# Optimization experiments

Hardware: AMD Instinct MI355X
Metric: run time of the kernel (lower is better)

The kernel has to match this reference:

```python
import jax, jax.numpy as jnp
import numpy as np

B, CIN, OUT = 16, 64, 64
CH = CIN // 2          # depthwise group count (32)
H, W = 256, 256        # mas resolution; cen is at (H//2, W//2)

# The 8 fixed 3x3 dilation-3 kernels are center-minus-shifted-neighbor ops.
# Cross-correlation offsets (dy, dx) of the -1 tap, dilation 3:
OFFSETS = [(-3, -3), (-3, 0), (-3, 3), (0, 3), (3, 3), (3, 0), (3, -3), (0, -3)]


def setup_inputs() -> dict:
    key = jax.random.key(0)
    ks = jax.random.split(key, 9)
    cen = jax.random.normal(ks[0], (B, CIN, H // 2, W // 2), jnp.float32)
    mas = jax.random.normal(ks[1], (B, CH, H, W), jnp.float32)
    # inp_layer: Conv2d(CH, CH, k=3, s=2, p=1) + SiLU
    w_inp = jax.random.normal(ks[2], (CH, CH, 3, 3), jnp.float32) * 0.05
    b_inp = jax.random.normal(ks[3], (CH,), jnp.float32) * 0.05
    # layer1/2/3: grouped 1x1, groups=CH, per-group 8 in -> 2 out; store as [CH, 2, 8]
    w1 = jax.random.normal(ks[4], (CH, 2, 8), jnp.float32) * 0.1
    w2 = jax.random.normal(ks[5], (CH, 2, 8), jnp.float32) * 0.1
    w3 = jax.random.normal(ks[6], (CH, 2, 8), jnp.float32) * 0.1
    # out_conv: 1x1 conv, 3*CIN -> OUT, with bias
    w_out = jax.random.normal(ks[7], (OUT, 3 * CIN), jnp.float32) * 0.05
    b_out = jax.random.normal(ks[8], (OUT,), jnp.float32) * 0.05
    return {"cen": cen, "mas": mas, "w_inp": w_inp, "b_inp": b_inp,
            "w1": w1, "w2": w2, "w3": w3, "w_out": w_out, "b_out": b_out}


def _forward(cen, mas, w_inp, b_inp, w1, w2, w3, w_out, b_out):
    # stem: 3x3 stride-2 conv + SiLU  -> [B, CH, H//2, W//2]
    x = jax.lax.conv_general_dilated(
        mas, w_inp, window_strides=(2, 2), padding=((1, 1), (1, 1)),
        dimension_numbers=("NCHW", "OIHW", "NCHW"))
    x = jax.nn.silu(x + b_inp[None, :, None, None])
    b, c, h, w = x.shape
    # 8 dilated depthwise diff-convs == center minus zero-padded shifted copy
    xp = jnp.pad(x, ((0, 0), (0, 0), (3, 3), (3, 3)))
    deltas = jnp.stack(
        [x - jax.lax.dynamic_slice(xp, (0, 0, 3 + dy, 3 + dx), (b, c, h, w))
         for dy, dx in OFFSETS], axis=2)                     # [B, CH, 8, h, w]
    # grouped 1x1 gating convs (groups=CH): per-group [2,8] matmul
    g1 = jnp.einsum("bcdhw,cod->bcohw", deltas, w1)
    g2 = jnp.einsum("bcdhw,cod->bcohw", deltas, w2)
    square = (g1 * g2).reshape(b, 2 * c, h, w)               # layer1 * layer2
    dout = jnp.einsum("bcdhw,cod->bcohw", deltas, w3).reshape(b, 2 * c, h, w)
    # concat [square, dout, cen] along channels -> 1x1 out_conv
    outs = jnp.concatenate([square, dout, cen], axis=1)      # [B, 3*CIN, h, w]
    return jnp.einsum("bchw,oc->bohw", outs, w_out) + b_out[None, :, None, None]


def reference(cen, mas, w_inp, b_inp, w1, w2, w3, w_out, b_out):
    return _forward(cen, mas, w_inp, b_inp, w1, w2, w3, w_out, b_out)
```

## Files before the change

kernel.cpp:

```cpp
#include <hip/hip_runtime.h>
#include <hip/hip_bf16.h>

#define BATCH 16
#define CH    32
#define CIN   64
#define OUTC  64
#define HH    128
#define WW    128
#define HW    (HH * WW)
#define MHW   65536

typedef __attribute__((ext_vector_type(8))) short bf16x8;
typedef __attribute__((ext_vector_type(4))) float f32x4;

__device__ inline unsigned short bf16u(float x) {
  union { __hip_bfloat16 h; unsigned short s; } u;
  u.h = __float2bfloat16(x);
  return u.s;
}
__device__ inline unsigned int pack2(float lo, float hi) {
  return (unsigned int)bf16u(lo) | ((unsigned int)bf16u(hi) << 16);
}
__device__ inline float losf(unsigned u) { return __uint_as_float(u << 16); }
__device__ inline float hisf(unsigned u) { return __uint_as_float(u & 0xffff0000u); }

__global__ __launch_bounds__(256) void k_prep_weights(
    const float* __restrict__ w_out, const float* __restrict__ w_inp,
    const float* __restrict__ w3,
    unsigned short* __restrict__ wfrag, unsigned short* __restrict__ wfrag2,
    unsigned short* __restrict__ wfrag3) {
  int t = blockIdx.x * 256 + threadIdx.x;
  if (t < 9 * 2 * 64 * 8) {
    int e    = t & 7;
    int lane = (t >> 3) & 63;
    int ct   = (t >> 9) & 1;
    int tap  = t >> 10;
    int co = ct * 16 + (lane & 15);
    int ci = (lane >> 4) * 8 + e;
    wfrag[t] = bf16u(w_inp[(co * CH + ci) * 9 + tap]);
  }
  int t2 = t - 9216;
  if (t2 >= 0 && t2 < 8192) {
    int e    = t2 & 7;
    int lane = (t2 >> 3) & 63;
    int ot   = (t2 >> 9) & 3;
    int kt   = t2 >> 11;
    int o = ot * 16 + (lane & 15);
    int k = kt * 32 + (lane >> 4) * 8 + e;
    int col = (k < 64) ? k : 64 + k;
    wfrag2[t2] = bf16u(w_out[o * 192 + col]);
  }
  int t3 = t - 17408;
  if (t3 >= 0 && t3 < 18432) {
    int e    = t3 & 7;
    int lane = (t3 >> 3) & 63;
    int ot   = (t3 >> 9) & 3;
    int tap  = t3 >> 11;
    int o = ot * 16 + (lane & 15);
    int C = (lane >> 4) * 8 + e;
    const int kmap[9] = {0, 1, 2, 7, -1, 3, 6, 5, 4};
    float v = 0.f;
    if (tap == 4) {
      for (int k = 0; k < 8; ++k)
        for (int op = 0; op < 2; ++op)
          v += w_out[o * 192 + 64 + 2 * C + op] * w3[C * 16 + op * 8 + k];
    } else {
      int k = kmap[tap];
      for (int op = 0; op < 2; ++op)
        v -= w_out[o * 192 + 64 + 2 * C + op] * w3[C * 16 + op * 8 + k];
    }
    wfrag3[t3] = bf16u(v);
  }
}

__global__ __launch_bounds__(256, 6) void k_stem(
    const float* __restrict__ mas, const unsigned short* __restrict__ wfrag,
    const float* __restrict__ b_inp, unsigned short* __restrict__ xbuf) {
  __shared__ alignas(16) unsigned int xs32[325 * 18];

  const int W = blockIdx.x + 4 * blockIdx.y + 256 * blockIdx.z;
  const int F = (W & 7) * 512 + (W >> 3);
  const int bx = F & 3;
  const int by = (F >> 2) & 63;
  const int b  = F >> 8;

  const int t  = threadIdx.x;
  const int lane = t & 63;
  const int w = t >> 6;

  const int I0 = by * 2, J0 = bx * 32;
  const int R0 = 4 * by - 1, C0 = 64 * bx - 1;

  const float* mb = mas + (size_t)b * CH * MHW;

  if (R0 >= 0) {
#pragma unroll 5
    for (int idx = t; idx < 2560; idx += 256) {
      int cell = idx >> 5;
      int k    = idx & 31;
      int r  = cell >> 4;
      int cp = cell & 15;
      const float* p = mb + (size_t)(2 * cp) * MHW +
                       (size_t)(R0 + r) * 256 + (C0 + 1 + 2 * k);
      float2 a = *(const float2*)(p);
      float2 c = *(const float2*)(p + MHW);
      int base = (r * 65 + 1 + 2 * k) * 18 + cp;
      xs32[base]      = pack2(a.x, c.x);
      xs32[base + 18] = pack2(a.y, c.y);
    }
  } else {
#pragma unroll 5
    for (int idx = t; idx < 2560; idx += 256) {
      int cell = idx >> 5;
      int k    = idx & 31;
      int r  = cell >> 4;
      int cp = cell & 15;
      int gr = R0 + r;
      unsigned v0 = 0u, v1 = 0u;
      if (gr >= 0) {
        const float* p = mb + (size_t)(2 * cp) * MHW + (size_t)gr * 256 +
                         (C0 + 1 + 2 * k);
        float2 a = *(const float2*)(p);
        float2 c = *(const float2*)(p + MHW);
        v0 = pack2(a.x, c.x);
        v1 = pack2(a.y, c.y);
      }
      int base = (r * 65 + 1 + 2 * k) * 18 + cp;
      xs32[base]      = v0;
      xs32[base + 18] = v1;
    }
  }
  if (t < 80) {
    int r = t >> 4, cp = t & 15;
    int gr = R0 + r;
    unsigned v = 0u;
    if (gr >= 0 && bx > 0) {
      const float* p = mb + (size_t)(2 * cp) * MHW + (size_t)gr * 256 + C0;
      v = pack2(p[0], p[MHW]);
    }
    xs32[(r * 65) * 18 + cp] = v;
  }
  __syncthreads();

  const int il = w >> 1, h = w & 1;
  const int jl = lane & 15;
  const int g4 = (lane >> 4) * 4;
  const int tc = h * 16 + jl;

  f32x4 acc[2];
  acc[0] = 0.f;
  acc[1] = 0.f;

  const bf16x8* wf = (const bf16x8*)wfrag;
#pragma unroll
  for (int ky = 0; ky < 3; ++ky) {
#pragma unroll
    for (int kx = 0; kx < 3; ++kx) {
      const int tap = ky * 3 + kx;
      bf16x8 a0 = wf[(tap * 2 + 0) * 64 + lane];
      bf16x8 a1 = wf[(tap * 2 + 1) * 64 + lane];
      int pix = (2 * il + ky) * 65 + 2 * tc + kx;
      bf16x8 bfr = *(const bf16x8*)(xs32 + pix * 18 + g4);
      acc[0] = __builtin_amdgcn_mfma_f32_16x16x32_bf16(a0, bfr, acc[0], 0, 0, 0);
      acc[1] = __builtin_amdgcn_mfma_f32_16x16x32_bf16(a1, bfr, acc[1], 0, 0, 0);
    }
  }

  float4 bia[2];
  bia[0] = *(const float4*)(b_inp + (lane >> 4) * 4);
  bia[1] = *(const float4*)(b_inp + 16 + (lane >> 4) * 4);
  const int colg = J0 + tc;
  const int i = I0 + il;
#pragma unroll
  for (int ct = 0; ct < 2; ++ct) {
    int co0 = ct * 16 + (lane >> 4) * 4;
    float y0 = acc[ct][0] + ((const float*)&bia[ct])[0];
    float y1 = acc[ct][1] + ((const float*)&bia[ct])[1];
    float y2 = acc[ct][2] + ((const float*)&bia[ct])[2];
    float y3 = acc[ct][3] + ((const float*)&bia[ct])[3];
    float s0 = y0 / (1.f + __expf(-y0));
    float s1 = y1 / (1.f + __expf(-y1));
    float s2 = y2 / (1.f + __expf(-y2));
    float s3 = y3 / (1.f + __expf(-y3));
    uint2 uv;
    uv.x = pack2(s0, s1);
    uv.y = pack2(s2, s3);
    *(uint2*)(xbuf + ((size_t)(b * HH + i) * WW + colg) * 32 + co0) = uv;
  }
}

#define PPITCH 132

__global__ __launch_bounds__(256, 4) void k_fused(
    const unsigned short* __restrict__ xbuf, const float* __restrict__ cen,
    const float* __restrict__ w1, const float* __restrict__ w2,
    const unsigned short* __restrict__ wfrag2,
    const unsigned short* __restrict__ wfrag3,
    const float* __restrict__ b_out, float* __restrict__ out) {
  __shared__ alignas(16) unsigned short xs[196 * 36];
  __shared__ alignas(16) unsigned short panel[64][PPITCH];

  const int W = blockIdx.x + 16 * blockIdx.y + 256 * blockIdx.z;
  const int F = (W & 7) * 512 + (W >> 3);
  const int bx = F & 15;
  const int by = (F >> 4) & 15;
  const int b  = F >> 8;

  const int t  = threadIdx.x;
  const int lane = t & 63;
  const int w = t >> 6;
  const int I0 = by * 8, J0 = bx * 8;

  bf16x8 af3[9], af2[4];
#pragma unroll
  for (int tap = 0; tap < 9; ++tap)
    af3[tap] = ((const bf16x8*)wfrag3)[(tap * 4 + w) * 64 + lane];
#pragma unroll
  for (int kt = 0; kt < 4; ++kt)
    af2[kt] = ((const bf16x8*)wfrag2)[(kt * 4 + w) * 64 + lane];

#pragma unroll
  for (int j = 0; j < 4; ++j) {
    int idx = j * 256 + t;
    int cc = idx >> 5;
    int pp = idx & 31;
    int p0 = 2 * pp;
    int py = p0 >> 3, px = p0 & 7;
    const float* cp = cen + ((size_t)(b * CIN + 2 * cc) * HH + I0 + py) * WW
                      + J0 + px;
    float2 a = *(const float2*)(cp);
    float2 c = *(const float2*)(cp + HW);
    *(unsigned int*)&panel[p0][64 + 2 * cc]     = pack2(a.x, c.x);
    *(unsigned int*)&panel[p0 + 1][64 + 2 * cc] = pack2(a.y, c.y);
  }

  {
    int row = t >> 4, col = t & 15;
    if (row < 14 && col < 14) {
      const bool interior = (bx >= 1 && bx <= 14 && by >= 1 && by <= 14);
      int gi = I0 - 3 + row, gj = J0 - 3 + col;
      unsigned short* sp = xs + (row * 14 + col) * 36;
      if (interior) {
        const unsigned short* gp = xbuf +
            ((size_t)((size_t)b * HH + gi) * WW + gj) * 32;
#pragma unroll
        for (int s = 0; s < 4; ++s) {
          uint4 v = *(const uint4*)(gp + 8 * s);
          *(uint2*)(sp + 8 * s)     = make_uint2(v.x, v.y);
          *(uint2*)(sp + 8 * s + 4) = make_uint2(v.z, v.w);
        }
      } else {
        bool ok = (gi >= 0 && gi < HH && gj >= 0 && gj < WW);
        const unsigned short* gp = xbuf +
            ((size_t)((size_t)b * HH + (ok ? gi : 0)) * WW + (ok ? gj : 0)) * 32;
#pragma unroll
        for (int s = 0; s < 4; ++s) {
          uint4 v = make_uint4(0u, 0u, 0u, 0u);
          if (ok) v = *(const uint4*)(gp + 8 * s);
          *(uint2*)(sp + 8 * s)     = make_uint2(v.x, v.y);
          *(uint2*)(sp + 8 * s + 4) = make_uint2(v.z, v.w);
        }
      }
    }
  }
  __syncthreads();

  f32x4 acc[4];
#pragma unroll
  for (int pt = 0; pt < 4; ++pt) acc[pt] = 0.f;

  const int prow = lane & 15;
  const int gsh = (lane >> 4) * 8;
#pragma unroll
  for (int pt = 0; pt < 4; ++pt) {
    int p = pt * 16 + prow;
    int ppy = p >> 3, ppx = p & 7;
#pragma unroll
    for (int ty = 0; ty < 3; ++ty)
#pragma unroll
      for (int tx = 0; tx < 3; ++tx) {
        int pos = (ppy + 3 * ty) * 14 + ppx + 3 * tx;
        bf16x8 bfr = *(const bf16x8*)(xs + pos * 36 + gsh);
        acc[pt] = __builtin_amdgcn_mfma_f32_16x16x32_bf16(
            af3[ty * 3 + tx], bfr, acc[pt], 0, 0, 0);
      }
  }

  {
    const int py = lane >> 3, px = lane & 7;
    const int posc = (py + 3) * 14 + (px + 3);
    int pos8[8];
    pos8[0] = (py + 0) * 14 + px + 0;
    pos8[1] = (py + 0) * 14 + px + 3;
    pos8[2] = (py + 0) * 14 + px + 6;
    pos8[3] = (py + 3) * 14 + px + 6;
    pos8[4] = (py + 6) * 14 + px + 6;
    pos8[5] = (py + 6) * 14 + px + 3;
    pos8[6] = (py + 6) * 14 + px + 0;
    pos8[7] = (py + 3) * 14 + px + 0;

#pragma unroll
    for (int j = 0; j < 4; ++j) {
      int c2 = __builtin_amdgcn_readfirstlane(j * 4 + w);
      const float* w1lo = w1 + (2 * c2) * 16;
      const float* w1hi = w1 + (2 * c2 + 1) * 16;
      const float* w2lo = w2 + (2 * c2) * 16;
      const float* w2hi = w2 + (2 * c2 + 1) * 16;
      unsigned uc = *(const unsigned*)(xs + posc * 36 + 2 * c2);
      float clo = losf(uc), chi = hisf(uc);
      float g1l0 = 0, g1l1 = 0, g2l0 = 0, g2l1 = 0;
      float g1h0 = 0, g1h1 = 0, g2h0 = 0, g2h1 = 0;
#pragma unroll
      for (int k = 0; k < 8; ++k) {
        unsigned us = *(const unsigned*)(xs + pos8[k] * 36 + 2 * c2);
        float dlo = clo - losf(us);
        float dhi = chi - hisf(us);
        g1l0 += dlo * w1lo[k];  g1l1 += dlo * w1lo[8 + k];
        g2l0 += dlo * w2lo[k];  g2l1 += dlo * w2lo[8 + k];
        g1h0 += dhi * w1hi[k];  g1h1 += dhi * w1hi[8 + k];
        g2h0 += dhi * w2hi[k];  g2h1 += dhi * w2hi[8 + k];
      }
      uint2 wv;
      wv.x = pack2(g1l0 * g2l0, g1l1 * g2l1);
      wv.y = pack2(g1h0 * g2h0, g1h1 * g2h1);
      *(uint2*)&panel[lane][4 * c2] = wv;
    }
  }
  __syncthreads();

#pragma unroll
  for (int pt = 0; pt < 4; ++pt) {
#pragma unroll
    for (int kt = 0; kt < 4; ++kt) {
      bf16x8 bfr = *(const bf16x8*)(&panel[pt * 16 + prow][kt * 32 + gsh]);
      acc[pt] = __builtin_amdgcn_mfma_f32_16x16x32_bf16(
          af2[kt], bfr, acc[pt], 0, 0, 0);
    }
  }

  float4 bo = *(const float4*)(b_out + w * 16 + (lane >> 4) * 4);
#pragma unroll
  for (int pt = 0; pt < 4; ++pt) {
    int p = pt * 16 + prow;
    int ppy = p >> 3, ppx = p & 7;
#pragma unroll
    for (int r = 0; r < 4; ++r) {
      int o = w * 16 + (lane >> 4) * 4 + r;
      out[((b * OUTC + o) * HH + I0 + ppy) * WW + J0 + ppx] =
          acc[pt][r] + ((const float*)&bo)[r];
    }
  }
}

extern "C" void kernel_launch(void* const* d_in, const int* in_sizes, int n_in,
                              void* d_out, int out_size, void* d_ws, size_t ws_size,
                              hipStream_t stream) {
  const float* cen   = (const float*)d_in[0];
  const float* mas   = (const float*)d_in[1];
  const float* w_inp = (const float*)d_in[2];
  const float* b_inp = (const float*)d_in[3];
  const float* w1    = (const float*)d_in[4];
  const float* w2    = (const float*)d_in[5];
  const float* w3    = (const float*)d_in[6];
  const float* w_out = (const float*)d_in[7];
  const float* b_out = (const float*)d_in[8];
  float* out = (float*)d_out;

  unsigned short* xbuf   = (unsigned short*)d_ws;
  unsigned short* wfrag  = xbuf + (size_t)BATCH * HW * 32;
  unsigned short* wfrag2 = wfrag + 9216;
  unsigned short* wfrag3 = wfrag2 + 8192;

  hipLaunchKernelGGL(k_prep_weights, dim3(140), dim3(256), 0, stream,
                     w_out, w_inp, w3, wfrag, wfrag2, wfrag3);
  hipLaunchKernelGGL(k_stem, dim3(4, 64, 16), dim3(256), 0, stream,
                     mas, wfrag, b_inp, xbuf);
  hipLaunchKernelGGL(k_fused, dim3(16, 16, 16), dim3(256), 0, stream,
                     xbuf, cen, w1, w2, wfrag2, wfrag3, b_out, out);
}
```

Before: 99.00 us.

## Reshape fused kernel tile to 4x16 pixels and deepen stem load unrolling

The fused kernel's per-block output tile changes from 8x8 to 4 rows by 16 columns. This gives wider contiguous rows for the cen loads (float4 instead of float2) and for the output stores (16 consecutive floats per row). The halo grows from 14x14 to 10x22 positions (196 to 220), so each block loads a bit more halo, and the halo load loop is redistributed across threads by segment. The stem load loop unroll factor also doubles from 5 to 10.

```diff
diff --git a/kernel.cpp b/kernel.cpp
--- a/kernel.cpp
+++ b/kernel.cpp
@@ -94,7 +94,7 @@
   const float* mb = mas + (size_t)b * CH * MHW;
 
   if (R0 >= 0) {
-#pragma unroll 5
+#pragma unroll 10
     for (int idx = t; idx < 2560; idx += 256) {
       int cell = idx >> 5;
       int k    = idx & 31;
@@ -109,7 +109,7 @@
       xs32[base + 18] = pack2(a.y, c.y);
     }
   } else {
-#pragma unroll 5
+#pragma unroll 10
     for (int idx = t; idx < 2560; idx += 256) {
       int cell = idx >> 5;
       int k    = idx & 31;
@@ -190,6 +190,7 @@
 }
 
 #define PPITCH 132
+#define HALOP 22
 
 __global__ __launch_bounds__(256, 4) void k_fused(
     const unsigned short* __restrict__ xbuf, const float* __restrict__ cen,
@@ -197,19 +198,19 @@
     const unsigned short* __restrict__ wfrag2,
     const unsigned short* __restrict__ wfrag3,
     const float* __restrict__ b_out, float* __restrict__ out) {
-  __shared__ alignas(16) unsigned short xs[196 * 36];
+  __shared__ alignas(16) unsigned short xs[220 * 36];
   __shared__ alignas(16) unsigned short panel[64][PPITCH];
 
-  const int W = blockIdx.x + 16 * blockIdx.y + 256 * blockIdx.z;
+  const int W = blockIdx.x + 8 * blockIdx.y + 256 * blockIdx.z;
   const int F = (W & 7) * 512 + (W >> 3);
-  const int bx = F & 15;
-  const int by = (F >> 4) & 15;
+  const int bx = F & 7;
+  const int by = (F >> 3) & 31;
   const int b  = F >> 8;
 
   const int t  = threadIdx.x;
   const int lane = t & 63;
   const int w = t >> 6;
-  const int I0 = by * 8, J0 = bx * 8;
+  const int I0 = by * 4, J0 = bx * 16;
 
   bf16x8 af3[9], af2[4];
 #pragma unroll
@@ -220,46 +221,43 @@
     af2[kt] = ((const bf16x8*)wfrag2)[(kt * 4 + w) * 64 + lane];
 
 #pragma unroll
-  for (int j = 0; j < 4; ++j) {
+  for (int j = 0; j < 2; ++j) {
     int idx = j * 256 + t;
-    int cc = idx >> 5;
-    int pp = idx & 31;
-    int p0 = 2 * pp;
-    int py = p0 >> 3, px = p0 & 7;
+    int cc = idx >> 4;
+    int q  = idx & 15;
+    int p0 = q * 4;
+    int py = p0 >> 4, px0 = p0 & 15;
     const float* cp = cen + ((size_t)(b * CIN + 2 * cc) * HH + I0 + py) * WW
-                      + J0 + px;
-    float2 a = *(const float2*)(cp);
-    float2 c = *(const float2*)(cp + HW);
+                      + J0 + px0;
+    float4 a = *(const float4*)(cp);
+    float4 c = *(const float4*)(cp + HW);
     *(unsigned int*)&panel[p0][64 + 2 * cc]     = pack2(a.x, c.x);
     *(unsigned int*)&panel[p0 + 1][64 + 2 * cc] = pack2(a.y, c.y);
+    *(unsigned int*)&panel[p0 + 2][64 + 2 * cc] = pack2(a.z, c.z);
+    *(unsigned int*)&panel[p0 + 3][64 + 2 * cc] = pack2(a.w, c.w);
   }
 
   {
-    int row = t >> 4, col = t & 15;
-    if (row < 14 && col < 14) {
-      const bool interior = (bx >= 1 && bx <= 14 && by >= 1 && by <= 14);
+    const bool interior = (bx >= 1 && bx <= 6 && by >= 1 && by <= 30);
+    for (int idx = t; idx < 880; idx += 256) {
+      int px = idx >> 2, seg = idx & 3;
+      int row = px / HALOP, col = px - row * HALOP;
       int gi = I0 - 3 + row, gj = J0 - 3 + col;
-      unsigned short* sp = xs + (row * 14 + col) * 36;
+      unsigned short* sp = xs + px * 36 + seg * 8;
       if (interior) {
         const unsigned short* gp = xbuf +
             ((size_t)((size_t)b * HH + gi) * WW + gj) * 32;
-#pragma unroll
-        for (int s = 0; s < 4; ++s) {
-          uint4 v = *(const uint4*)(gp + 8 * s);
-          *(uint2*)(sp + 8 * s)     = make_uint2(v.x, v.y);
-          *(uint2*)(sp + 8 * s + 4) = make_uint2(v.z, v.w);
-        }
+        uint4 v = *(const uint4*)(gp + 8 * seg);
+        *(uint2*)(sp)     = make_uint2(v.x, v.y);
+        *(uint2*)(sp + 4) = make_uint2(v.z, v.w);
       } else {
         bool ok = (gi >= 0 && gi < HH && gj >= 0 && gj < WW);
         const unsigned short* gp = xbuf +
             ((size_t)((size_t)b * HH + (ok ? gi : 0)) * WW + (ok ? gj : 0)) * 32;
-#pragma unroll
-        for (int s = 0; s < 4; ++s) {
-          uint4 v = make_uint4(0u, 0u, 0u, 0u);
-          if (ok) v = *(const uint4*)(gp + 8 * s);
-          *(uint2*)(sp + 8 * s)     = make_uint2(v.x, v.y);
-          *(uint2*)(sp + 8 * s + 4) = make_uint2(v.z, v.w);
-        }
+        uint4 v = make_uint4(0u, 0u, 0u, 0u);
+        if (ok) v = *(const uint4*)(gp + 8 * seg);
+        *(uint2*)(sp)     = make_uint2(v.x, v.y);
+        *(uint2*)(sp + 4) = make_uint2(v.z, v.w);
       }
     }
   }
@@ -273,13 +271,11 @@
   const int gsh = (lane >> 4) * 8;
 #pragma unroll
   for (int pt = 0; pt < 4; ++pt) {
-    int p = pt * 16 + prow;
-    int ppy = p >> 3, ppx = p & 7;
 #pragma unroll
     for (int ty = 0; ty < 3; ++ty)
 #pragma unroll
       for (int tx = 0; tx < 3; ++tx) {
-        int pos = (ppy + 3 * ty) * 14 + ppx + 3 * tx;
+        int pos = (pt + 3 * ty) * HALOP + prow + 3 * tx;
         bf16x8 bfr = *(const bf16x8*)(xs + pos * 36 + gsh);
         acc[pt] = __builtin_amdgcn_mfma_f32_16x16x32_bf16(
             af3[ty * 3 + tx], bfr, acc[pt], 0, 0, 0);
@@ -287,17 +283,17 @@
   }
 
   {
-    const int py = lane >> 3, px = lane & 7;
-    const int posc = (py + 3) * 14 + (px + 3);
+    const int py = lane >> 4, px = lane & 15;
+    const int posc = (py + 3) * HALOP + (px + 3);
     int pos8[8];
-    pos8[0] = (py + 0) * 14 + px + 0;
-    pos8[1] = (py + 0) * 14 + px + 3;
-    pos8[2] = (py + 0) * 14 + px + 6;
-    pos8[3] = (py + 3) * 14 + px + 6;
-    pos8[4] = (py + 6) * 14 + px + 6;
-    pos8[5] = (py + 6) * 14 + px + 3;
-    pos8[6] = (py + 6) * 14 + px + 0;
-    pos8[7] = (py + 3) * 14 + px + 0;
+    pos8[0] = (py + 0) * HALOP + px + 0;
+    pos8[1] = (py + 0) * HALOP + px + 3;
+    pos8[2] = (py + 0) * HALOP + px + 6;
+    pos8[3] = (py + 3) * HALOP + px + 6;
+    pos8[4] = (py + 6) * HALOP + px + 6;
+    pos8[5] = (py + 6) * HALOP + px + 3;
+    pos8[6] = (py + 6) * HALOP + px + 0;
+    pos8[7] = (py + 3) * HALOP + px + 0;
 
 #pragma unroll
     for (int j = 0; j < 4; ++j) {
@@ -341,12 +337,10 @@
   float4 bo = *(const float4*)(b_out + w * 16 + (lane >> 4) * 4);
 #pragma unroll
   for (int pt = 0; pt < 4; ++pt) {
-    int p = pt * 16 + prow;
-    int ppy = p >> 3, ppx = p & 7;
 #pragma unroll
     for (int r = 0; r < 4; ++r) {
       int o = w * 16 + (lane >> 4) * 4 + r;
-      out[((b * OUTC + o) * HH + I0 + ppy) * WW + J0 + ppx] =
+      out[((b * OUTC + o) * HH + I0 + pt) * WW + J0 + prow] =
           acc[pt][r] + ((const float*)&bo)[r];
     }
   }
@@ -375,6 +369,6 @@
                      w_out, w_inp, w3, wfrag, wfrag2, wfrag3);
   hipLaunchKernelGGL(k_stem, dim3(4, 64, 16), dim3(256), 0, stream,
                      mas, wfrag, b_inp, xbuf);
-  hipLaunchKernelGGL(k_fused, dim3(16, 16, 16), dim3(256), 0, stream,
+  hipLaunchKernelGGL(k_fused, dim3(8, 32, 16), dim3(256), 0, stream,
                      xbuf, cen, w1, w2, wfrag2, wfrag3, b_out, out);
 }
```

After: 96.50 us. 2.5% less time.
